# Kernel optimization log

Measured on AMD Instinct MI355X. Metric: run time of the kernel, lower is better.

The kernel has to match this reference:

```python
import jax, jax.numpy as jnp
import numpy as np

B, L, D, K = 4, 512, 768, 96
H = 4 * D  # projection hidden width


def _proj(x, w1, b1, w2, b2):
    # create_projection_layer: Linear -> ReLU -> (Dropout, identity at eval) -> Linear
    return jnp.maximum(x @ w1 + b1, 0.0) @ w2 + b2


def setup_inputs() -> dict:
    key = jax.random.key(0)
    ks = jax.random.split(key, 12)
    g = lambda k, shape, fan: jax.random.normal(k, shape, jnp.float32) * (1.0 / np.sqrt(fan))
    inp = {
        "h": jax.random.normal(ks[0], (B, L, D), jnp.float32),
        "span_idx": jax.random.randint(ks[1], (B, K, 2), 0, L),
        "ps_w1": g(ks[2], (D, H), D), "ps_b1": jnp.zeros((H,), jnp.float32),
        "ps_w2": g(ks[3], (H, D), H), "ps_b2": jnp.zeros((D,), jnp.float32),
        "pe_w1": g(ks[4], (D, H), D), "pe_b1": jnp.zeros((H,), jnp.float32),
        "pe_w2": g(ks[5], (H, D), H), "pe_b2": jnp.zeros((D,), jnp.float32),
        "so_w1": g(ks[6], (2 * D, H), 2 * D), "so_b1": jnp.zeros((H,), jnp.float32),
        "so_w2": g(ks[7], (H, D), H), "so_b2": jnp.zeros((D,), jnp.float32),
        "ro_w1": g(ks[8], (2 * D, H), 2 * D), "ro_b1": jnp.zeros((H,), jnp.float32),
        "ro_w2": g(ks[9], (H, D), H), "ro_b2": jnp.zeros((D,), jnp.float32),
    }
    return inp


def _gather_tokens(rep, idx):
    # rep: [B,L,D], idx: [B,K] -> [B,K,D]
    b, k = idx.shape
    d = rep.shape[-1]
    return jnp.take_along_axis(rep, jnp.broadcast_to(idx[:, :, None], (b, k, d)), axis=1)


def reference(h, span_idx, ps_w1, ps_b1, ps_w2, ps_b2, pe_w1, pe_b1, pe_w2, pe_b2,
              so_w1, so_b1, so_w2, so_b2, ro_w1, ro_b1, ro_w2, ro_b2):
    # SpanMarkerV1
    start_rep = _proj(h, ps_w1, ps_b1, ps_w2, ps_b2)   # [B,L,D]
    end_rep = _proj(h, pe_w1, pe_b1, pe_w2, pe_b2)     # [B,L,D]
    st = _gather_tokens(start_rep, span_idx[:, :, 0])  # [B,K,D]
    en = _gather_tokens(end_rep, span_idx[:, :, 1])    # [B,K,D]
    cat = jnp.maximum(jnp.concatenate([st, en], axis=-1), 0.0)  # relu
    entity_reps = _proj(cat, so_w1, so_b1, so_w2, so_b2)        # [B,K,D]

    # off-diagonal pair enumeration, row-major (i,j) with i != j — static indices
    n = entity_reps.shape[1]
    idx = np.arange(n)
    ii = np.repeat(idx, n)
    jj = np.tile(idx, n)
    keep = ii != jj
    ii, jj = ii[keep], jj[keep]  # each length n*(n-1)
    pairs = jnp.concatenate([entity_reps[:, ii], entity_reps[:, jj]], axis=-1)  # [B,P,2D]
    return _proj(pairs, ro_w1, ro_b1, ro_w2, ro_b2)  # [B,P,D]
```

## Files before the change

kernel.cpp:

```cpp
#include <hip/hip_runtime.h>
#include <hip/hip_bf16.h>

#define Bdim 4
#define Ldim 512
#define Ddim 768
#define Kspan 96
#define Hdim 3072
#define Pdim 9120
#define MROWS 384
#define NT 48

typedef __bf16 bf16x8 __attribute__((ext_vector_type(8)));
typedef float f32x4 __attribute__((ext_vector_type(4)));
typedef float f32x16 __attribute__((ext_vector_type(16)));
typedef unsigned short ushort8v __attribute__((ext_vector_type(8)));

static __device__ __forceinline__ unsigned short f2bf(float x){
  return __builtin_bit_cast(unsigned short, (__bf16)x);
}
static __device__ __forceinline__ float bf2f(unsigned short u){
  return (float)__builtin_bit_cast(__bf16, u);
}

__global__ __launch_bounds__(256) void transpose_split(
    const float* __restrict__ W, unsigned short* __restrict__ WTh,
    unsigned short* __restrict__ WTl, int K, int N)
{
  __shared__ float tile[64][65];
  int k0 = blockIdx.y * 64, n0 = blockIdx.x * 64;
  int c = threadIdx.x & 63, r0 = threadIdx.x >> 6;
  for (int p = 0; p < 16; p++){
    int r = r0 + p * 4;
    tile[c][r] = W[(size_t)(k0 + r) * N + n0 + c];
  }
  __syncthreads();
  for (int p = 0; p < 16; p++){
    int n = r0 + p * 4;
    float x = tile[n][c];
    unsigned short h = f2bf(x);
    size_t o = (size_t)(n0 + n) * K + k0 + c;
    WTh[o] = h;
    WTl[o] = f2bf(x - bf2f(h));
  }
}

__global__ __launch_bounds__(256) void transpose_cvt_swz(
    const float* __restrict__ W, unsigned short* __restrict__ WT, int K, int N)
{
  __shared__ float tile[64][65];
  int k0 = blockIdx.y * 64, n0 = blockIdx.x * 64;
  int c = threadIdx.x & 63, r0 = threadIdx.x >> 6;
  for (int p = 0; p < 16; p++){
    int r = r0 + p * 4;
    tile[c][r] = W[(size_t)(k0 + r) * N + n0 + c];
  }
  __syncthreads();
  for (int p = 0; p < 16; p++){
    int n = r0 + p * 4;
    int nrow = n0 + n;
    int kk = k0 + c;
    int gq = (kk >> 3) & 7, e = kk & 7;
    int kph = (kk & ~63) | ((gq ^ (nrow & 7)) << 3) | e;
    WT[(size_t)nrow * K + kph] = f2bf(tile[n][c]);
  }
}

__global__ __launch_bounds__(256) void gather_rows(
    const float* __restrict__ h, const int* __restrict__ span, float* __restrict__ hg)
{
  int x = blockIdx.x;
  int sel = (x >= MROWS) ? 1 : 0;
  int r = x - sel * MROWS;
  int b = r / Kspan, k = r - b * Kspan;
  int idx = span[(b * Kspan + k) * 2 + sel];
  const float* src = h + ((size_t)b * Ldim + idx) * Ddim;
  float* dst = hg + (size_t)x * Ddim;
  for (int d = threadIdx.x; d < Ddim; d += 256) dst[d] = src[d];
}

struct GJob {
  const float* A;
  const unsigned short* Wh;
  const unsigned short* Wl;
  const float* bias;
  float* C;
};

template<int MODE, int SPLIT>
__global__ __launch_bounds__(256) void gemm_ms(
    GJob j0, GJob j1, int ldA, int ldW, int ldC, int kLen, size_t csz)
{
  constexpr int SR = 40;
  __shared__ __align__(16) unsigned short Ah[64 * SR], Al[64 * SR];
  __shared__ __align__(16) unsigned short Bh[128 * SR], Bl[128 * SR];
  int zj, s;
  if (SPLIT == 1){ zj = blockIdx.z; s = 0; }
  else { zj = blockIdx.z / SPLIT; s = blockIdx.z % SPLIT; }
  const GJob J = zj ? j1 : j0;
  int kBegin = s * kLen;
  float* Cptr = (MODE == 2) ? (J.C + (size_t)s * csz) : J.C;

  int m0 = blockIdx.y * 64, n0 = blockIdx.x * 128;
  int t = threadIdx.x, lane = t & 63, wid = t >> 6;
  int wm = wid >> 1, wn = wid & 1;
  int lr = lane & 15, lk = (lane >> 4) * 8;
  f32x4 acc[2][4] = {};
  int ar = t >> 2, akq = t & 3;
  for (int k0 = 0; k0 < kLen; k0 += 32){
    {
      const float* sp = J.A + (size_t)(m0 + ar) * ldA + kBegin + k0 + akq * 8;
      f32x4 x0 = *(const f32x4*)sp, x1 = *(const f32x4*)(sp + 4);
      ushort8v vh, vl;
      for (int e = 0; e < 4; e++){ float x = x0[e]; unsigned short hh = f2bf(x); vh[e] = hh; vl[e] = f2bf(x - bf2f(hh)); }
      for (int e = 0; e < 4; e++){ float x = x1[e]; unsigned short hh = f2bf(x); vh[e+4] = hh; vl[e+4] = f2bf(x - bf2f(hh)); }
      *(ushort8v*)&Ah[ar * SR + akq * 8] = vh;
      *(ushort8v*)&Al[ar * SR + akq * 8] = vl;
    }
    for (int p = 0; p < 2; p++){
      int idx = p * 256 + t; int n = idx >> 2, kq = idx & 3;
      size_t go = (size_t)(n0 + n) * ldW + kBegin + k0 + kq * 8;
      *(ushort8v*)&Bh[n * SR + kq * 8] = *(const ushort8v*)(J.Wh + go);
      *(ushort8v*)&Bl[n * SR + kq * 8] = *(const ushort8v*)(J.Wl + go);
    }
    __syncthreads();
    bf16x8 ah[2], al2[2], bh[4], bl[4];
    for (int f = 0; f < 2; f++){ int o = (wm * 32 + f * 16 + lr) * SR + lk; ah[f] = *(const bf16x8*)&Ah[o]; al2[f] = *(const bf16x8*)&Al[o]; }
    for (int g = 0; g < 4; g++){ int o = (wn * 64 + g * 16 + lr) * SR + lk; bh[g] = *(const bf16x8*)&Bh[o]; bl[g] = *(const bf16x8*)&Bl[o]; }
    for (int f = 0; f < 2; f++)
      for (int g = 0; g < 4; g++){
        acc[f][g] = __builtin_amdgcn_mfma_f32_16x16x32_bf16(ah[f],  bh[g], acc[f][g], 0, 0, 0);
        acc[f][g] = __builtin_amdgcn_mfma_f32_16x16x32_bf16(ah[f],  bl[g], acc[f][g], 0, 0, 0);
        acc[f][g] = __builtin_amdgcn_mfma_f32_16x16x32_bf16(al2[f], bh[g], acc[f][g], 0, 0, 0);
      }
    __syncthreads();
  }
  int rr = (lane >> 4) * 4;
  for (int f = 0; f < 2; f++){
    int gm = m0 + wm * 32 + f * 16 + rr;
    for (int g = 0; g < 4; g++){
      int gn = n0 + wn * 64 + g * 16 + (lane & 15);
      float bv = (MODE != 2 && J.bias) ? J.bias[gn] : 0.f;
      for (int r2 = 0; r2 < 4; r2++){
        float v = acc[f][g][r2] + bv;
        if (MODE == 0) v = fmaxf(v, 0.f);
        Cptr[(size_t)(gm + r2) * ldC + gn] = v;
      }
    }
  }
}

template<bool RELU>
__global__ __launch_bounds__(256) void reduce_part(
    const float* __restrict__ P, int S,
    const float* __restrict__ bias0, const float* __restrict__ bias1,
    float* __restrict__ outp, int zCount, int ldOut)
{
  const int MN = MROWS * Ddim;
  int idx4 = blockIdx.x * 256 + threadIdx.x;
  int flat = idx4 * 4;
  if (flat >= MN * zCount) return;
  int z = flat / MN; int rem = flat - z * MN;
  int r = rem / Ddim; int c = rem - r * Ddim;
  const float* base = P + (size_t)z * S * MN + rem;
  f32x4 sv = *(const f32x4*)base;
  for (int ss = 1; ss < S; ss++){ f32x4 v = *(const f32x4*)(base + (size_t)ss * MN); sv += v; }
  const float* bp = z ? bias1 : bias0;
  f32x4 bv = *(const f32x4*)(bp + c);
  sv += bv;
  if (RELU) for (int e = 0; e < 4; e++) sv[e] = fmaxf(sv[e], 0.f);
  *(f32x4*)(outp + (size_t)r * ldOut + z * Ddim + c) = sv;
}

__global__ __launch_bounds__(256) void pair_gemm2(
    const float* __restrict__ U,
    const float* __restrict__ V,
    const unsigned short* __restrict__ W2Ts,
    const float* __restrict__ b2,
    float* __restrict__ out)
{
  __shared__ __align__(16) unsigned short Bs[2][384 * 64];
  __shared__ __align__(16) unsigned short As[2][96 * 64];

  int x = blockIdx.x;
  int xcd = x & 7, i = x >> 3;
  int half = xcd >> 2;
  int b = xcd & 3;

  const float* Urow = U + ((size_t)b * Kspan + i) * Hdim;
  const float* Vb   = V + (size_t)b * Kspan * Hdim;
  const unsigned short* Wp = W2Ts + (size_t)half * 384 * Hdim;

  int t = threadIdx.x, lane = t & 63, w = t >> 6;
  int kq = t & 7, r0a = t >> 3;

  float ureg[8];
  float vreg[3][8];
  f32x16 acc[3][3] = {};

  auto issueB = [&](int tt, int buf){
    const unsigned short* wkp = Wp + tt * 64;
    unsigned int* ldsbase = (unsigned int*)&Bs[buf][0];
    int c0 = w * 12;
    #pragma unroll
    for (int q = 0; q < 12; q++){
      int row = (c0 + q) * 8 + (lane >> 3);
      const unsigned short* src = wkp + (size_t)row * Hdim + (lane & 7) * 8;
      unsigned int* dst = ldsbase + ((c0 + q) * 256 + lane * 4);
      __builtin_amdgcn_global_load_lds(
          (const __attribute__((address_space(1))) unsigned int*)src,
          (__attribute__((address_space(3))) unsigned int*)dst, 16, 0, 0);
    }
  };
  auto issueA = [&](int tt){
    const float* up = Urow + tt * 64 + kq * 8;
    *(f32x4*)&ureg[0] = *(const f32x4*)up;
    *(f32x4*)&ureg[4] = *(const f32x4*)(up + 4);
    #pragma unroll
    for (int it = 0; it < 3; it++){
      const float* vp = Vb + (size_t)(r0a + 32 * it) * Hdim + tt * 64 + kq * 8;
      *(f32x4*)&vreg[it][0] = *(const f32x4*)vp;
      *(f32x4*)&vreg[it][4] = *(const f32x4*)(vp + 4);
    }
  };
  auto writeA = [&](int buf){
    #pragma unroll
    for (int it = 0; it < 3; it++){
      int r = r0a + 32 * it;
      ushort8v pk;
      #pragma unroll
      for (int e = 0; e < 8; e++) pk[e] = f2bf(fmaxf(ureg[e] + vreg[it][e], 0.f));
      *(ushort8v*)((char*)&As[buf][0] + r * 128 + ((kq ^ (r & 7)) * 16)) = pk;
    }
  };
  auto mfmaPhase = [&](int buf){
    #pragma unroll
    for (int kh = 0; kh < 4; kh++){
      int gg = kh * 2 + (lane >> 5);
      bf16x8 af[3], bfr[3];
      #pragma unroll
      for (int mf = 0; mf < 3; mf++){
        int r = mf * 32 + (lane & 31);
        af[mf] = *(const bf16x8*)((const char*)&As[buf][0] + r * 128 + ((gg ^ (r & 7)) * 16));
      }
      #pragma unroll
      for (int nf = 0; nf < 3; nf++){
        int n = w * 96 + nf * 32 + (lane & 31);
        bfr[nf] = *(const bf16x8*)((const char*)&Bs[buf][0] + n * 128 + ((gg ^ (n & 7)) * 16));
      }
      __builtin_amdgcn_s_setprio(1);
      #pragma unroll
      for (int mf = 0; mf < 3; mf++)
        #pragma unroll
        for (int nf = 0; nf < 3; nf++)
          acc[mf][nf] = __builtin_amdgcn_mfma_f32_32x32x16_bf16(af[mf], bfr[nf], acc[mf][nf], 0, 0, 0);
      __builtin_amdgcn_s_setprio(0);
    }
  };

  issueB(0, 0);
  issueA(0);
  writeA(0);
  __syncthreads();

  for (int tt = 0; tt < NT; tt++){
    int cur = tt & 1;
    if (tt + 1 < NT){ issueB(tt + 1, cur ^ 1); issueA(tt + 1); }
    mfmaPhase(cur);
    if (tt + 1 < NT) writeA(cur ^ 1);
    __syncthreads();
  }

  size_t outB = (size_t)b * Pdim;
  int colbase = half * 384 + w * 96;
  float bc[3];
  #pragma unroll
  for (int nf = 0; nf < 3; nf++) bc[nf] = b2[colbase + nf * 32 + (lane & 31)];
  #pragma unroll
  for (int mf = 0; mf < 3; mf++){
    #pragma unroll
    for (int reg = 0; reg < 16; reg++){
      int j = mf * 32 + (reg & 3) + 8 * (reg >> 2) + 4 * (lane >> 5);
      if (j == i) continue;
      int p = i * 95 + j - (j > i ? 1 : 0);
      float* orow = out + (outB + p) * Ddim + colbase;
      #pragma unroll
      for (int nf = 0; nf < 3; nf++){
        int cn = nf * 32 + (lane & 31);
        orow[cn] = acc[mf][nf][reg] + bc[nf];
      }
    }
  }
}

extern "C" void kernel_launch(void* const* d_in, const int* in_sizes, int n_in,
                              void* d_out, int out_size, void* d_ws, size_t ws_size,
                              hipStream_t stream)
{
  (void)in_sizes; (void)n_in; (void)out_size;
  const float* h     = (const float*)d_in[0];
  const int*   span  = (const int*)d_in[1];
  const float* ps_w1 = (const float*)d_in[2];
  const float* ps_b1 = (const float*)d_in[3];
  const float* ps_w2 = (const float*)d_in[4];
  const float* ps_b2 = (const float*)d_in[5];
  const float* pe_w1 = (const float*)d_in[6];
  const float* pe_b1 = (const float*)d_in[7];
  const float* pe_w2 = (const float*)d_in[8];
  const float* pe_b2 = (const float*)d_in[9];
  const float* so_w1 = (const float*)d_in[10];
  const float* so_b1 = (const float*)d_in[11];
  const float* so_w2 = (const float*)d_in[12];
  const float* so_b2 = (const float*)d_in[13];
  const float* ro_w1 = (const float*)d_in[14];
  const float* ro_b1 = (const float*)d_in[15];
  const float* ro_w2 = (const float*)d_in[16];
  const float* ro_b2 = (const float*)d_in[17];

  char* ws = (char*)d_ws;
  size_t off = 0;
  auto alloc_us = [&](size_t n)->unsigned short*{
    unsigned short* p = (unsigned short*)(ws + off);
    off += ((n * 2 + 255) & ~(size_t)255);
    return p;
  };
  auto alloc_f = [&](size_t n)->float*{
    float* p = (float*)(ws + off);
    off += ((n * 4 + 255) & ~(size_t)255);
    return p;
  };

  unsigned short* ps1h = alloc_us((size_t)Hdim * Ddim); unsigned short* ps1l = alloc_us((size_t)Hdim * Ddim);
  unsigned short* ps2h = alloc_us((size_t)Ddim * Hdim); unsigned short* ps2l = alloc_us((size_t)Ddim * Hdim);
  unsigned short* pe1h = alloc_us((size_t)Hdim * Ddim); unsigned short* pe1l = alloc_us((size_t)Hdim * Ddim);
  unsigned short* pe2h = alloc_us((size_t)Ddim * Hdim); unsigned short* pe2l = alloc_us((size_t)Ddim * Hdim);
  unsigned short* so1h = alloc_us((size_t)Hdim * 2 * Ddim); unsigned short* so1l = alloc_us((size_t)Hdim * 2 * Ddim);
  unsigned short* so2h = alloc_us((size_t)Ddim * Hdim); unsigned short* so2l = alloc_us((size_t)Ddim * Hdim);
  unsigned short* ro1h = alloc_us((size_t)Hdim * 2 * Ddim); unsigned short* ro1l = alloc_us((size_t)Hdim * 2 * Ddim);
  unsigned short* ro2Ts = alloc_us((size_t)Ddim * Hdim);
  float* hg     = alloc_f((size_t)2 * MROWS * Ddim);
  float* mid_s  = alloc_f((size_t)MROWS * Hdim);
  float* mid_e  = alloc_f((size_t)MROWS * Hdim);
  float* cat    = alloc_f((size_t)MROWS * 2 * Ddim);
  float* entity = alloc_f((size_t)MROWS * Ddim);
  float* Ubuf   = alloc_f((size_t)MROWS * Hdim);
  float* Vbuf   = alloc_f((size_t)MROWS * Hdim);
  const size_t MN = (size_t)MROWS * Ddim;
  float* P2 = alloc_f(8 * MN);
  float* P3 = alloc_f(4 * MN);
  if (off > ws_size) return;

  dim3 tb(256);
  transpose_split<<<dim3(Hdim/64, Ddim/64), tb, 0, stream>>>(ps_w1, ps1h, ps1l, Ddim, Hdim);
  transpose_split<<<dim3(Ddim/64, Hdim/64), tb, 0, stream>>>(ps_w2, ps2h, ps2l, Hdim, Ddim);
  transpose_split<<<dim3(Hdim/64, Ddim/64), tb, 0, stream>>>(pe_w1, pe1h, pe1l, Ddim, Hdim);
  transpose_split<<<dim3(Ddim/64, Hdim/64), tb, 0, stream>>>(pe_w2, pe2h, pe2l, Hdim, Ddim);
  transpose_split<<<dim3(Hdim/64, (2*Ddim)/64), tb, 0, stream>>>(so_w1, so1h, so1l, 2*Ddim, Hdim);
  transpose_split<<<dim3(Ddim/64, Hdim/64), tb, 0, stream>>>(so_w2, so2h, so2l, Hdim, Ddim);
  transpose_split<<<dim3(Hdim/64, (2*Ddim)/64), tb, 0, stream>>>(ro_w1, ro1h, ro1l, 2*Ddim, Hdim);
  transpose_cvt_swz<<<dim3(Ddim/64, Hdim/64), tb, 0, stream>>>(ro_w2, ro2Ts, Hdim, Ddim);

  gather_rows<<<2 * MROWS, tb, 0, stream>>>(h, span, hg);

  {
    GJob j0{hg,                      ps1h, ps1l, ps_b1, mid_s};
    GJob j1{hg + (size_t)MROWS*Ddim, pe1h, pe1l, pe_b1, mid_e};
    gemm_ms<0,1><<<dim3(Hdim/128, MROWS/64, 2), tb, 0, stream>>>(j0, j1, Ddim, Ddim, Hdim, Ddim, 0);
  }
  {
    GJob j0{mid_s, ps2h, ps2l, nullptr, P2};
    GJob j1{mid_e, pe2h, pe2l, nullptr, P2 + 4*MN};
    gemm_ms<2,4><<<dim3(Ddim/128, MROWS/64, 8), tb, 0, stream>>>(j0, j1, Hdim, Hdim, Ddim, Hdim/4, MN);
  }
  reduce_part<true><<<(2*(int)MN)/1024, tb, 0, stream>>>(P2, 4, ps_b2, pe_b2, cat, 2, 2*Ddim);
  {
    GJob j0{cat, so1h, so1l, so_b1, mid_s};
    gemm_ms<0,1><<<dim3(Hdim/128, MROWS/64, 1), tb, 0, stream>>>(j0, j0, 2*Ddim, 2*Ddim, Hdim, 2*Ddim, 0);
  }
  {
    GJob j0{mid_s, so2h, so2l, nullptr, P3};
    gemm_ms<2,4><<<dim3(Ddim/128, MROWS/64, 4), tb, 0, stream>>>(j0, j0, Hdim, Hdim, Ddim, Hdim/4, MN);
  }
  reduce_part<false><<<((int)MN)/1024, tb, 0, stream>>>(P3, 4, so_b2, so_b2, entity, 1, Ddim);
  {
    GJob j0{entity, ro1h,        ro1l,        ro_b1,   Ubuf};
    GJob j1{entity, ro1h + Ddim, ro1l + Ddim, nullptr, Vbuf};
    gemm_ms<1,1><<<dim3(Hdim/128, MROWS/64, 2), tb, 0, stream>>>(j0, j1, Ddim, 2*Ddim, Hdim, Ddim, 0);
  }

  pair_gemm2<<<Bdim * Kspan * 2, tb, 0, stream>>>(Ubuf, Vbuf, ro2Ts, ro_b2, (float*)d_out);
}
```

Measured before the change: 538.8 us.

## Retile pair GEMM to four query rows per block with packed bf16 V and W2

The final pair GEMM is restructured. Each block now computes 4 query entities × 96 partners (384 M rows) against a 96-column slice of W2, instead of 1 query × 96 partners against 384 columns. The K tile shrinks to 32 and launch bounds allow 2 blocks per CU. New pack kernels pre-tile W2 and V into bf16 K-tile-contiguous layouts so each tile is one contiguous load, and the LDS buffers are smaller. This gives more reuse of each W2 tile across rows and cuts fp32 V reads, at the cost of an extra pack pass, double the K iterations and a different swizzle.

```diff
diff --git a/kernel.cpp b/kernel.cpp
--- a/kernel.cpp
+++ b/kernel.cpp
@@ -8,12 +8,13 @@
 #define Hdim 3072
 #define Pdim 9120
 #define MROWS 384
-#define NT 48
+#define NKT 96
 
 typedef __bf16 bf16x8 __attribute__((ext_vector_type(8)));
 typedef float f32x4 __attribute__((ext_vector_type(4)));
 typedef float f32x16 __attribute__((ext_vector_type(16)));
 typedef unsigned short ushort8v __attribute__((ext_vector_type(8)));
+typedef unsigned short ushort4v __attribute__((ext_vector_type(4)));
 
 static __device__ __forceinline__ unsigned short f2bf(float x){
   return __builtin_bit_cast(unsigned short, (__bf16)x);
@@ -44,24 +45,35 @@
   }
 }
 
-__global__ __launch_bounds__(256) void transpose_cvt_swz(
-    const float* __restrict__ W, unsigned short* __restrict__ WT, int K, int N)
-{
-  __shared__ float tile[64][65];
-  int k0 = blockIdx.y * 64, n0 = blockIdx.x * 64;
-  int c = threadIdx.x & 63, r0 = threadIdx.x >> 6;
-  for (int p = 0; p < 16; p++){
-    int r = r0 + p * 4;
-    tile[c][r] = W[(size_t)(k0 + r) * N + n0 + c];
+__global__ __launch_bounds__(256) void pack_w2(
+    const float* __restrict__ W, unsigned short* __restrict__ W2P)
+{
+  __shared__ float tile[32][97];
+  int kt = blockIdx.x, nq = blockIdx.y, t = threadIdx.x;
+  for (int q = 0; q < 12; q++){
+    int flat = q * 256 + t;
+    int kl = flat / 96, n = flat - kl * 96;
+    tile[kl][n] = W[(size_t)(kt * 32 + kl) * Ddim + nq * 96 + n];
   }
   __syncthreads();
-  for (int p = 0; p < 16; p++){
-    int n = r0 + p * 4;
-    int nrow = n0 + n;
-    int kk = k0 + c;
-    int gq = (kk >> 3) & 7, e = kk & 7;
-    int kph = (kk & ~63) | ((gq ^ (nrow & 7)) << 3) | e;
-    WT[(size_t)nrow * K + kph] = f2bf(tile[n][c]);
+  unsigned short* outp = W2P + ((size_t)(nq * 96 + kt)) * 3072;
+  for (int q = 0; q < 12; q++){
+    int o = q * 256 + t;
+    int n = o >> 5, klx = o & 31;
+    int kl = klx ^ ((n & 8) << 1);
+    outp[o] = f2bf(tile[kl][n]);
+  }
+}
+
+__global__ __launch_bounds__(256) void pack_v(
+    const float* __restrict__ Vbuf, unsigned short* __restrict__ Vp)
+{
+  int kt = blockIdx.x, b = blockIdx.y, t = threadIdx.x;
+  unsigned short* outp = Vp + ((size_t)(b * 96 + kt)) * 3072;
+  for (int q = 0; q < 12; q++){
+    int flat = q * 256 + t;
+    int j = flat >> 5, kl = flat & 31;
+    outp[flat] = f2bf(Vbuf[(size_t)(b * 96 + j) * Hdim + kt * 32 + kl]);
   }
 }
 
@@ -171,81 +183,85 @@
   *(f32x4*)(outp + (size_t)r * ldOut + z * Ddim + c) = sv;
 }
 
-__global__ __launch_bounds__(256) void pair_gemm2(
+__global__ __launch_bounds__(256, 2) void pair_gemm3(
     const float* __restrict__ U,
-    const float* __restrict__ V,
-    const unsigned short* __restrict__ W2Ts,
+    const unsigned short* __restrict__ Vp,
+    const unsigned short* __restrict__ W2P,
     const float* __restrict__ b2,
     float* __restrict__ out)
 {
-  __shared__ __align__(16) unsigned short Bs[2][384 * 64];
-  __shared__ __align__(16) unsigned short As[2][96 * 64];
+  __shared__ __align__(16) unsigned short As[2][384 * 32];
+  __shared__ __align__(16) unsigned short Bs[2][96 * 32];
 
   int x = blockIdx.x;
-  int xcd = x & 7, i = x >> 3;
-  int half = xcd >> 2;
-  int b = xcd & 3;
-
-  const float* Urow = U + ((size_t)b * Kspan + i) * Hdim;
-  const float* Vb   = V + (size_t)b * Kspan * Hdim;
-  const unsigned short* Wp = W2Ts + (size_t)half * 384 * Hdim;
+  int nq = x & 7;
+  int l = x >> 3;
+  int b = l / 24;
+  int iq = l - b * 24;
 
   int t = threadIdx.x, lane = t & 63, w = t >> 6;
-  int kq = t & 7, r0a = t >> 3;
-
-  float ureg[8];
-  float vreg[3][8];
+  int kq = t & 7, jb = t >> 3;
+
+  ushort4v vld[3];
+  f32x4 uld[4];
   f32x16 acc[3][3] = {};
 
-  auto issueB = [&](int tt, int buf){
-    const unsigned short* wkp = Wp + tt * 64;
-    unsigned int* ldsbase = (unsigned int*)&Bs[buf][0];
-    int c0 = w * 12;
-    #pragma unroll
-    for (int q = 0; q < 12; q++){
-      int row = (c0 + q) * 8 + (lane >> 3);
-      const unsigned short* src = wkp + (size_t)row * Hdim + (lane & 7) * 8;
-      unsigned int* dst = ldsbase + ((c0 + q) * 256 + lane * 4);
-      __builtin_amdgcn_global_load_lds(
-          (const __attribute__((address_space(1))) unsigned int*)src,
-          (__attribute__((address_space(3))) unsigned int*)dst, 16, 0, 0);
-    }
-  };
-  auto issueA = [&](int tt){
-    const float* up = Urow + tt * 64 + kq * 8;
-    *(f32x4*)&ureg[0] = *(const f32x4*)up;
-    *(f32x4*)&ureg[4] = *(const f32x4*)(up + 4);
-    #pragma unroll
-    for (int it = 0; it < 3; it++){
-      const float* vp = Vb + (size_t)(r0a + 32 * it) * Hdim + tt * 64 + kq * 8;
-      *(f32x4*)&vreg[it][0] = *(const f32x4*)vp;
-      *(f32x4*)&vreg[it][4] = *(const f32x4*)(vp + 4);
-    }
-  };
-  auto writeA = [&](int buf){
-    #pragma unroll
-    for (int it = 0; it < 3; it++){
-      int r = r0a + 32 * it;
-      ushort8v pk;
-      #pragma unroll
-      for (int e = 0; e < 8; e++) pk[e] = f2bf(fmaxf(ureg[e] + vreg[it][e], 0.f));
-      *(ushort8v*)((char*)&As[buf][0] + r * 128 + ((kq ^ (r & 7)) * 16)) = pk;
+  auto issueB = [&](int kt, int buf){
+    const unsigned short* tb = W2P + ((size_t)(nq * 96 + kt)) * 3072;
+    #pragma unroll
+    for (int s2 = 0; s2 < 2; s2++){
+      int seg = w + s2 * 4;
+      if (seg < 6){
+        const unsigned short* src = tb + seg * 512 + lane * 8;
+        unsigned int* dst = (unsigned int*)&Bs[buf][seg * 512 + lane * 8];
+        __builtin_amdgcn_global_load_lds(
+            (const __attribute__((address_space(1))) unsigned int*)src,
+            (__attribute__((address_space(3))) unsigned int*)dst, 16, 0, 0);
+      }
+    }
+  };
+  auto issueUV = [&](int kt){
+    const unsigned short* vb = Vp + ((size_t)(b * 96 + kt)) * 3072 + kq * 4;
+    #pragma unroll
+    for (int q = 0; q < 3; q++)
+      vld[q] = *(const ushort4v*)(vb + (q * 32 + jb) * 32);
+    const float* ub = U + ((size_t)(b * 96 + iq * 4)) * Hdim + kt * 32 + kq * 4;
+    #pragma unroll
+    for (int g = 0; g < 4; g++)
+      uld[g] = *(const f32x4*)(ub + (size_t)g * Hdim);
+  };
+  auto buildA = [&](int buf){
+    #pragma unroll
+    for (int q = 0; q < 3; q++){
+      int j = q * 32 + jb;
+      f32x4 vf;
+      #pragma unroll
+      for (int e = 0; e < 4; e++) vf[e] = bf2f(vld[q][e]);
+      #pragma unroll
+      for (int g = 0; g < 4; g++){
+        int row = g * 96 + j;
+        ushort4v pk;
+        #pragma unroll
+        for (int e = 0; e < 4; e++) pk[e] = f2bf(fmaxf(uld[g][e] + vf[e], 0.f));
+        int idx = row * 32 + ((kq * 4) ^ ((row & 8) << 1));
+        *(ushort4v*)&As[buf][idx] = pk;
+      }
     }
   };
   auto mfmaPhase = [&](int buf){
     #pragma unroll
-    for (int kh = 0; kh < 4; kh++){
+    for (int kh = 0; kh < 2; kh++){
       int gg = kh * 2 + (lane >> 5);
       bf16x8 af[3], bfr[3];
       #pragma unroll
       for (int mf = 0; mf < 3; mf++){
-        int r = mf * 32 + (lane & 31);
-        af[mf] = *(const bf16x8*)((const char*)&As[buf][0] + r * 128 + ((gg ^ (r & 7)) * 16));
+        int row = w * 96 + mf * 32 + (lane & 31);
+        af[mf] = *(const bf16x8*)&As[buf][row * 32 + ((gg * 8) ^ ((row & 8) << 1))];
       }
       #pragma unroll
       for (int nf = 0; nf < 3; nf++){
-        int n = w * 96 + nf * 32 + (lane & 31);
-        bfr[nf] = *(const bf16x8*)((const char*)&Bs[buf][0] + n * 128 + ((gg ^ (n & 7)) * 16));
+        int n = nf * 32 + (lane & 31);
+        bfr[nf] = *(const bf16x8*)&Bs[buf][n * 32 + ((gg * 8) ^ ((n & 8) << 1))];
       }
       __builtin_amdgcn_s_setprio(1);
       #pragma unroll
@@ -258,20 +274,21 @@
   };
 
   issueB(0, 0);
-  issueA(0);
-  writeA(0);
+  issueUV(0);
+  buildA(0);
   __syncthreads();
 
-  for (int tt = 0; tt < NT; tt++){
-    int cur = tt & 1;
-    if (tt + 1 < NT){ issueB(tt + 1, cur ^ 1); issueA(tt + 1); }
+  for (int kt = 0; kt < NKT; kt++){
+    int cur = kt & 1;
+    if (kt + 1 < NKT){ issueB(kt + 1, cur ^ 1); issueUV(kt + 1); }
     mfmaPhase(cur);
-    if (tt + 1 < NT) writeA(cur ^ 1);
+    if (kt + 1 < NKT) buildA(cur ^ 1);
     __syncthreads();
   }
 
+  int i = iq * 4 + w;
   size_t outB = (size_t)b * Pdim;
-  int colbase = half * 384 + w * 96;
+  int colbase = nq * 96;
   float bc[3];
   #pragma unroll
   for (int nf = 0; nf < 3; nf++) bc[nf] = b2[colbase + nf * 32 + (lane & 31)];
@@ -336,7 +353,8 @@
   unsigned short* so1h = alloc_us((size_t)Hdim * 2 * Ddim); unsigned short* so1l = alloc_us((size_t)Hdim * 2 * Ddim);
   unsigned short* so2h = alloc_us((size_t)Ddim * Hdim); unsigned short* so2l = alloc_us((size_t)Ddim * Hdim);
   unsigned short* ro1h = alloc_us((size_t)Hdim * 2 * Ddim); unsigned short* ro1l = alloc_us((size_t)Hdim * 2 * Ddim);
-  unsigned short* ro2Ts = alloc_us((size_t)Ddim * Hdim);
+  unsigned short* W2P  = alloc_us((size_t)Ddim * Hdim);
+  unsigned short* Vp   = alloc_us((size_t)Bdim * Kspan * Hdim);
   float* hg     = alloc_f((size_t)2 * MROWS * Ddim);
   float* mid_s  = alloc_f((size_t)MROWS * Hdim);
   float* mid_e  = alloc_f((size_t)MROWS * Hdim);
@@ -357,7 +375,7 @@
   transpose_split<<<dim3(Hdim/64, (2*Ddim)/64), tb, 0, stream>>>(so_w1, so1h, so1l, 2*Ddim, Hdim);
   transpose_split<<<dim3(Ddim/64, Hdim/64), tb, 0, stream>>>(so_w2, so2h, so2l, Hdim, Ddim);
   transpose_split<<<dim3(Hdim/64, (2*Ddim)/64), tb, 0, stream>>>(ro_w1, ro1h, ro1l, 2*Ddim, Hdim);
-  transpose_cvt_swz<<<dim3(Ddim/64, Hdim/64), tb, 0, stream>>>(ro_w2, ro2Ts, Hdim, Ddim);
+  pack_w2<<<dim3(NKT, 8), tb, 0, stream>>>(ro_w2, W2P);
 
   gather_rows<<<2 * MROWS, tb, 0, stream>>>(h, span, hg);
 
@@ -386,6 +404,7 @@
     GJob j1{entity, ro1h + Ddim, ro1l + Ddim, nullptr, Vbuf};
     gemm_ms<1,1><<<dim3(Hdim/128, MROWS/64, 2), tb, 0, stream>>>(j0, j1, Ddim, 2*Ddim, Hdim, Ddim, 0);
   }
-
-  pair_gemm2<<<Bdim * Kspan * 2, tb, 0, stream>>>(Ubuf, Vbuf, ro2Ts, ro_b2, (float*)d_out);
-}
+  pack_v<<<dim3(NKT, Bdim), tb, 0, stream>>>(Vbuf, Vp);
+
+  pair_gemm3<<<768, tb, 0, stream>>>(Ubuf, Vp, W2P, ro_b2, (float*)d_out);
+}
```

Result: no change. 531.1 us (-1.4%).
